# Performance work log

Hardware: AMD Instinct MI355X
Metric: run time of the kernel (lower is better)

The kernel has to match this reference:

```python
import jax, jax.numpy as jnp
import numpy as np

B, S, E, H = 4, 2048, 1024, 16
DK = E // H

def setup_inputs() -> dict:
    key = jax.random.key(0)
    ks = jax.random.split(key, 5)
    scale = 1.0 / np.sqrt(E)
    return {
        "x":  jax.random.normal(ks[0], (B, S, E), dtype=jnp.float32),
        "Wq": jax.random.normal(ks[1], (E, E), dtype=jnp.float32) * scale,
        "Wk": jax.random.normal(ks[2], (E, E), dtype=jnp.float32) * scale,
        "Wv": jax.random.normal(ks[3], (E, E), dtype=jnp.float32) * scale,
        "Wo": jax.random.normal(ks[4], (E, E), dtype=jnp.float32) * scale,
    }

def reference(x, Wq, Wk, Wv, Wo):
    b, s, e = x.shape
    # nn.Linear (no bias): y = x @ W.T
    def split_heads(t):  # (b, s, e) -> (b, H, s, DK)
        return t.reshape(b, s, H, DK).transpose(0, 2, 1, 3)
    Q = split_heads(x @ Wq.T)
    K = split_heads(x @ Wk.T)
    V = split_heads(x @ Wv.T)
    scores = jnp.einsum('bhqd,bhkd->bhqk', Q, K) / jnp.sqrt(jnp.float32(DK))
    attn = jax.nn.softmax(scores, axis=-1)  # dropout p=0.0 -> identity
    ctx = jnp.einsum('bhqk,bhkd->bhqd', attn, V)
    concat = ctx.transpose(0, 2, 1, 3).reshape(b, s, e)
    return concat @ Wo.T
```

## Files before the change

### kernel.cpp

```cpp
#include <hip/hip_runtime.h>


typedef __bf16 bf16x8 __attribute__((ext_vector_type(8)));
typedef __bf16 bf16x4 __attribute__((ext_vector_type(4)));
typedef float floatx4 __attribute__((ext_vector_type(4)));

#define GLOAD_LDS16(gp, lp) __builtin_amdgcn_global_load_lds( \
    (const __attribute__((address_space(1))) unsigned int*)(gp), \
    (__attribute__((address_space(3))) unsigned int*)(lp), 16, 0, 0)

__global__ __launch_bounds__(256) void cvt_x(const float4* __restrict__ s,
                                             bf16x4* __restrict__ d, int n4) {
    int i = blockIdx.x * 256 + threadIdx.x;
    if (i < n4) {
        float4 v = s[i];
        bf16x4 o = { (__bf16)v.x, (__bf16)v.y, (__bf16)v.z, (__bf16)v.w };
        d[i] = o;
    }
}

__global__ __launch_bounds__(256) void cvt_w(const float4* __restrict__ Wq,
                                             const float4* __restrict__ Wk,
                                             const float4* __restrict__ Wv,
                                             const float4* __restrict__ Wo,
                                             bf16x4* __restrict__ oq, bf16x4* __restrict__ ok,
                                             bf16x4* __restrict__ ov, bf16x4* __restrict__ oo,
                                             float qscale) {
    int y = blockIdx.y;
    const float4* s = (y == 0) ? Wq : (y == 1) ? Wk : (y == 2) ? Wv : Wo;
    bf16x4* d = (y == 0) ? oq : (y == 1) ? ok : (y == 2) ? ov : oo;
    float scale = (y == 0) ? qscale : 1.0f;
    int i = blockIdx.x * 256 + threadIdx.x;
    float4 v = s[i];
    bf16x4 o = { (__bf16)(v.x * scale), (__bf16)(v.y * scale),
                 (__bf16)(v.z * scale), (__bf16)(v.w * scale) };
    d[i] = o;
}


__device__ __forceinline__ void gemm_stage(const __bf16* __restrict__ A,
                                           const __bf16* __restrict__ W,
                                           __bf16* Asm, __bf16* Bsm,
                                           int bm, int bn, int k0, int w, int lane) {
#pragma unroll
    for (int j = 0; j < 2; ++j) {
        int base = j * 256 + w * 64;
        int flat = base + lane;
        int c = flat >> 7, r = flat & 127;
        GLOAD_LDS16(A + (size_t)(bm + r) * 1024 + k0 + c * 8, (char*)Asm + base * 16);
    }
#pragma unroll
    for (int j = 0; j < 4; ++j) {
        int base = j * 256 + w * 64;
        int flat = base + lane;
        int c = flat >> 8, r = flat & 255;
        GLOAD_LDS16(W + (size_t)(bn + r) * 1024 + k0 + c * 8, (char*)Bsm + base * 16);
    }
}

__device__ __forceinline__ void gemm_phase(const __bf16* __restrict__ A,
                                           const __bf16* __restrict__ W,
                                           const __bf16* Asm_r, const __bf16* Bsm_r,
                                           __bf16* Asm_s, __bf16* Bsm_s,
                                           int bm, int bn, int ks,
                                           int w, int lane, int quad, int l15,
                                           int wy, int wx,
                                           floatx4 acc[4][8]) {
    gemm_stage(A, W, Asm_s, Bsm_s, bm, bn, ks, w, lane);
    __builtin_amdgcn_sched_barrier(0);
    asm volatile("s_waitcnt vmcnt(6)" ::: "memory");
    __builtin_amdgcn_s_barrier();
    __builtin_amdgcn_sched_barrier(0);

    bf16x8 af[4], bf[8];
#pragma unroll
    for (int mt = 0; mt < 4; ++mt)
        af[mt] = *(const bf16x8*)(Asm_r + (quad * 128 + wy * 64 + mt * 16 + l15) * 8);
#pragma unroll
    for (int nt = 0; nt < 8; ++nt)
        bf[nt] = *(const bf16x8*)(Bsm_r + (quad * 256 + wx * 128 + nt * 16 + l15) * 8);
#pragma unroll
    for (int mt = 0; mt < 4; ++mt)
#pragma unroll
        for (int nt = 0; nt < 8; ++nt)
            acc[mt][nt] = __builtin_amdgcn_mfma_f32_16x16x32_bf16(af[mt], bf[nt],
                                                                  acc[mt][nt], 0, 0, 0);
    __builtin_amdgcn_sched_barrier(0);
    __builtin_amdgcn_s_barrier();
}

__device__ __forceinline__ void gemm_mainloop2(const __bf16* __restrict__ A,
                                               const __bf16* __restrict__ W,
                                               __bf16* SM,
                                               int bm, int bn, int tid,
                                               floatx4 acc[4][8]) {
    const int w = tid >> 6, lane = tid & 63;
    const int quad = lane >> 4, l15 = lane & 15;
    const int wy = w >> 1, wx = w & 1;
    __bf16* Asm0 = SM;
    __bf16* Bsm0 = SM + 4096;
    __bf16* Asm1 = SM + 12288;
    __bf16* Bsm1 = SM + 16384;
#pragma unroll
    for (int i = 0; i < 4; ++i)
#pragma unroll
        for (int j = 0; j < 8; ++j) acc[i][j] = (floatx4){0.f, 0.f, 0.f, 0.f};

    gemm_stage(A, W, Asm0, Bsm0, bm, bn, 0, w, lane);

    for (int k0 = 0; k0 < 1024; k0 += 64) {
        gemm_phase(A, W, Asm0, Bsm0, Asm1, Bsm1, bm, bn, k0 + 32,
                   w, lane, quad, l15, wy, wx, acc);
        gemm_phase(A, W, Asm1, Bsm1, Asm0, Bsm0, bm, bn, k0 + 64,
                   w, lane, quad, l15, wy, wx, acc);
    }
    __syncthreads();
}

__global__ __launch_bounds__(256, 2) void gemm_qkv(const __bf16* __restrict__ A,
                                                   const __bf16* __restrict__ Wqb,
                                                   const __bf16* __restrict__ Wkb,
                                                   const __bf16* __restrict__ Wvb,
                                                   __bf16* __restrict__ Qg,
                                                   __bf16* __restrict__ Kg,
                                                   __bf16* __restrict__ Vtg) {
    __shared__ alignas(16) __bf16 SM[24576];
    const int sel = blockIdx.x >> 2;
    const __bf16* W = (sel == 0) ? Wqb : (sel == 1) ? Wkb : Wvb;
    __bf16* ob = (sel == 0) ? Qg : (sel == 1) ? Kg : Vtg;
    const int bm = blockIdx.y * 128, bn = (blockIdx.x & 3) * 256;
    const int tid = threadIdx.x;
    const int w = tid >> 6, lane = tid & 63;
    const int quad = lane >> 4, l15 = lane & 15;
    const int wy = w >> 1, wx = w & 1;

    floatx4 acc[4][8];
    gemm_mainloop2(A, W, SM, bm, bn, tid, acc);

    float* tb = (float*)SM + w * 272;
    const int rr = lane >> 2, c0 = (lane & 3) * 4;
#pragma unroll
    for (int mt = 0; mt < 4; ++mt)
#pragma unroll
        for (int nt = 0; nt < 8; ++nt) {
            if (sel == 2) {
#pragma unroll
                for (int r = 0; r < 4; ++r) tb[l15 * 17 + quad * 4 + r] = acc[mt][nt][r];
            } else {
#pragma unroll
                for (int r = 0; r < 4; ++r) tb[(quad * 4 + r) * 17 + l15] = acc[mt][nt][r];
            }
            float f0 = tb[rr * 17 + c0 + 0], f1 = tb[rr * 17 + c0 + 1];
            float f2 = tb[rr * 17 + c0 + 2], f3 = tb[rr * 17 + c0 + 3];
            bf16x4 pk = { (__bf16)f0, (__bf16)f1, (__bf16)f2, (__bf16)f3 };
            if (sel <= 1) {
                int m = bm + wy * 64 + mt * 16 + rr;
                int n0 = bn + wx * 128 + nt * 16 + c0;
                int bI = m >> 11, s = m & 2047, h = n0 >> 6, d0 = n0 & 63;
                *(bf16x4*)(ob + ((size_t)(bI * 16 + h) * 2048 + s) * 64 + d0) = pk;
            } else {
                int m0 = bm + wy * 64 + mt * 16 + c0;
                int n = bn + wx * 128 + nt * 16 + rr;
                int bI = m0 >> 11, s0 = m0 & 2047, h = n >> 6, d = n & 63;
                *(bf16x4*)(ob + ((size_t)(bI * 16 + h) * 64 + d) * 2048 + s0) = pk;
            }
        }
}

__global__ __launch_bounds__(256, 2) void gemm_out(const __bf16* __restrict__ A,
                                                   const __bf16* __restrict__ W,
                                                   float* __restrict__ of) {
    __shared__ alignas(16) __bf16 SM[24576];
    const int tid = threadIdx.x;
    const int lane = tid & 63, w = tid >> 6;
    const int quad = lane >> 4, l15 = lane & 15;
    const int wy = w >> 1, wx = w & 1;
    const int bm = blockIdx.y * 128, bn = blockIdx.x * 256;

    floatx4 acc[4][8];
    gemm_mainloop2(A, W, SM, bm, bn, tid, acc);

#pragma unroll
    for (int mt = 0; mt < 4; ++mt)
#pragma unroll
        for (int nt = 0; nt < 8; ++nt)
#pragma unroll
            for (int r = 0; r < 4; ++r) {
                int m = bm + wy * 64 + mt * 16 + quad * 4 + r;
                int n = bn + wx * 128 + nt * 16 + l15;
                of[(size_t)m * 1024 + n] = acc[mt][nt][r];
            }
}


__device__ __forceinline__ int paddr(int c, int row) {
    int r2 = row ^ (((row >> 3) & 1) << 1) ^ (c & 1);
    return (c * 32 + r2) * 16;
}

__global__ __launch_bounds__(256, 4) void attn_kernel(const __bf16* __restrict__ Qg,
                                                      const __bf16* __restrict__ Kg,
                                                      const __bf16* __restrict__ Vtg,
                                                      __bf16* __restrict__ ctxg) {
    __shared__ alignas(16) __bf16 Ksm[4096];
    __shared__ alignas(16) __bf16 Vsm[4096];
    __shared__ alignas(16) __bf16 Psm[8192];
    const int tid = threadIdx.x;
    const int w = tid >> 6, lane = tid & 63;
    const int quad = lane >> 4, l15 = lane & 15;
    const int qbase = blockIdx.x * 128;
    const int bh = blockIdx.y;

    char* Pw = (char*)Psm + w * 4096;

    bf16x8 qf[2][2];
#pragma unroll
    for (int mt = 0; mt < 2; ++mt) {
        const __bf16* qrow = Qg + ((size_t)bh * 2048 + qbase + w * 32 + mt * 16 + l15) * 64;
        qf[mt][0] = *(const bf16x8*)(qrow + quad * 8);
        qf[mt][1] = *(const bf16x8*)(qrow + 32 + quad * 8);
    }

    float l_p[2][4] = {{0.f, 0.f, 0.f, 0.f}, {0.f, 0.f, 0.f, 0.f}};
    floatx4 o[2][4];
#pragma unroll
    for (int mt = 0; mt < 2; ++mt)
#pragma unroll
        for (int dt = 0; dt < 4; ++dt) o[mt][dt] = (floatx4){0.f, 0.f, 0.f, 0.f};

    for (int kv = 0; kv < 32; ++kv) {
        const int kv0 = kv * 64;
        __syncthreads();
#pragma unroll
        for (int j = 0; j < 2; ++j) {
            int base = j * 256 + w * 64;
            int flat = base + lane;
            int c = flat >> 6, r = flat & 63;
            GLOAD_LDS16(Kg + ((size_t)bh * 2048 + kv0 + r) * 64 + c * 8, (char*)Ksm + base * 16);
            GLOAD_LDS16(Vtg + ((size_t)bh * 64 + r) * 2048 + kv0 + c * 8, (char*)Vsm + base * 16);
        }
        __syncthreads();

        floatx4 sa[2][4];
#pragma unroll
        for (int mt = 0; mt < 2; ++mt)
#pragma unroll
            for (int nt = 0; nt < 4; ++nt) sa[mt][nt] = (floatx4){0.f, 0.f, 0.f, 0.f};
#pragma unroll
        for (int nt = 0; nt < 4; ++nt) {
            bf16x8 kb0 = *(const bf16x8*)(Ksm + (quad * 64 + nt * 16 + l15) * 8);
            bf16x8 kb1 = *(const bf16x8*)(Ksm + ((4 + quad) * 64 + nt * 16 + l15) * 8);
#pragma unroll
            for (int mt = 0; mt < 2; ++mt) {
                sa[mt][nt] = __builtin_amdgcn_mfma_f32_16x16x32_bf16(qf[mt][0], kb0,
                                                                    sa[mt][nt], 0, 0, 0);
                sa[mt][nt] = __builtin_amdgcn_mfma_f32_16x16x32_bf16(qf[mt][1], kb1,
                                                                    sa[mt][nt], 0, 0, 0);
            }
        }

#pragma unroll
        for (int mt = 0; mt < 2; ++mt)
#pragma unroll
            for (int nt = 0; nt < 4; ++nt)
#pragma unroll
                for (int r = 0; r < 4; ++r) {
                    float p = __builtin_amdgcn_exp2f(sa[mt][nt][r]);
                    l_p[mt][r] += p;
                    unsigned u = __builtin_bit_cast(unsigned, p);
                    *(unsigned short*)(Pw + paddr(nt * 2 + (l15 >> 3),
                                                  mt * 16 + quad * 4 + r)
                                       + (l15 & 7) * 2) = (unsigned short)(u >> 16);
                }

#pragma unroll
        for (int kk = 0; kk < 2; ++kk) {
            bf16x8 pa0 = *(const bf16x8*)(Pw + paddr(kk * 4 + quad, l15));
            bf16x8 pa1 = *(const bf16x8*)(Pw + paddr(kk * 4 + quad, 16 + l15));
#pragma unroll
            for (int dt = 0; dt < 4; ++dt) {
                bf16x8 vb = *(const bf16x8*)(Vsm + ((kk * 4 + quad) * 64 + dt * 16 + l15) * 8);
                o[0][dt] = __builtin_amdgcn_mfma_f32_16x16x32_bf16(pa0, vb, o[0][dt], 0, 0, 0);
                o[1][dt] = __builtin_amdgcn_mfma_f32_16x16x32_bf16(pa1, vb, o[1][dt], 0, 0, 0);
            }
        }
    }

    __syncthreads();

    float inv[2][4];
#pragma unroll
    for (int mt = 0; mt < 2; ++mt)
#pragma unroll
        for (int r = 0; r < 4; ++r) {
            float t = l_p[mt][r];
            t += __shfl_xor(t, 1); t += __shfl_xor(t, 2);
            t += __shfl_xor(t, 4); t += __shfl_xor(t, 8);
            inv[mt][r] = 1.f / t;
        }

    float* tb = (float*)Ksm + w * 272;
    const int bI = bh >> 4, h = bh & 15;
    const int rr = lane >> 2, c0 = (lane & 3) * 4;
#pragma unroll
    for (int mt = 0; mt < 2; ++mt)
#pragma unroll
        for (int dt = 0; dt < 4; ++dt) {
#pragma unroll
            for (int r = 0; r < 4; ++r)
                tb[(quad * 4 + r) * 17 + l15] = o[mt][dt][r] * inv[mt][r];
            float f0 = tb[rr * 17 + c0 + 0], f1 = tb[rr * 17 + c0 + 1];
            float f2 = tb[rr * 17 + c0 + 2], f3 = tb[rr * 17 + c0 + 3];
            bf16x4 pk = { (__bf16)f0, (__bf16)f1, (__bf16)f2, (__bf16)f3 };
            *(bf16x4*)(ctxg + ((size_t)(bI * 2048 + qbase + w * 32 + mt * 16 + rr)) * 1024
                       + h * 64 + dt * 16 + c0) = pk;
        }
}

extern "C" void kernel_launch(void* const* d_in, const int* in_sizes, int n_in,
                              void* d_out, int out_size, void* d_ws, size_t ws_size,
                              hipStream_t stream) {
    const float* x  = (const float*)d_in[0];
    const float* Wq = (const float*)d_in[1];
    const float* Wk = (const float*)d_in[2];
    const float* Wv = (const float*)d_in[3];
    const float* Wo = (const float*)d_in[4];
    float* out = (float*)d_out;
    char* ws = (char*)d_ws;

    __bf16* xb  = (__bf16*)(ws);
    __bf16* wqb = (__bf16*)(ws + (16u << 20));
    __bf16* wkb = (__bf16*)(ws + (18u << 20));
    __bf16* wvb = (__bf16*)(ws + (20u << 20));
    __bf16* wob = (__bf16*)(ws + (22u << 20));
    __bf16* Qg  = (__bf16*)(ws + (24u << 20));
    __bf16* Kg  = (__bf16*)(ws + (40u << 20));
    __bf16* Vtg = (__bf16*)(ws + (56u << 20));
    __bf16* ctx = xb;

    const float qscale = 0.18033688011112042f;

    cvt_x<<<8192, 256, 0, stream>>>((const float4*)x, (bf16x4*)xb, 2097152);
    cvt_w<<<dim3(1024, 4), 256, 0, stream>>>((const float4*)Wq, (const float4*)Wk,
                                             (const float4*)Wv, (const float4*)Wo,
                                             (bf16x4*)wqb, (bf16x4*)wkb,
                                             (bf16x4*)wvb, (bf16x4*)wob, qscale);

    gemm_qkv<<<dim3(12, 64), 256, 0, stream>>>(xb, wqb, wkb, wvb, Qg, Kg, Vtg);

    attn_kernel<<<dim3(16, 64), 256, 0, stream>>>(Qg, Kg, Vtg, ctx);

    gemm_out<<<dim3(4, 64), 256, 0, stream>>>(ctx, wob, out);
}
```

Baseline: 310.9 us.

## Double-buffer K/V tiles in attention and remap blocks across XCDs

The attention kernel now uses two LDS buffers for K and V. Each iteration prefetches the next tile with async global-to-LDS loads while it computes on the current one, synchronised by a vmcnt wait and a raw s_barrier, replacing the load-then-sync loop. The grid is flattened to 1D and block indices are permuted so that the query blocks of one head are grouped onto the same XCD, which should improve L2 reuse of K/V. LDS use grows, so occupancy drops from 4 to 3 blocks per CU. The last phase issues a redundant wrap-around prefetch of tile 0.

Result: no change. 309.9 us (-0.3%).

```diff
diff --git a/kernel.cpp b/kernel.cpp
--- a/kernel.cpp
+++ b/kernel.cpp
@@ -198,18 +198,98 @@
     return (c * 32 + r2) * 16;
 }
 
-__global__ __launch_bounds__(256, 4) void attn_kernel(const __bf16* __restrict__ Qg,
+__device__ __forceinline__ void attn_stage(const __bf16* __restrict__ Kg,
+                                           const __bf16* __restrict__ Vtg,
+                                           __bf16* Ks, __bf16* Vs,
+                                           int bh, int kv0, int w, int lane) {
+#pragma unroll
+    for (int j = 0; j < 2; ++j) {
+        int base = j * 256 + w * 64;
+        int flat = base + lane;
+        int c = flat >> 6, r = flat & 63;
+        GLOAD_LDS16(Kg + ((size_t)bh * 2048 + kv0 + r) * 64 + c * 8, (char*)Ks + base * 16);
+        GLOAD_LDS16(Vtg + ((size_t)bh * 64 + r) * 2048 + kv0 + c * 8, (char*)Vs + base * 16);
+    }
+}
+
+__device__ __forceinline__ void attn_phase(const __bf16* __restrict__ Kg,
+                                           const __bf16* __restrict__ Vtg,
+                                           const __bf16* Ksr, const __bf16* Vsr,
+                                           __bf16* Kss, __bf16* Vss,
+                                           char* Pw, const bf16x8 qf[2][2],
+                                           int bh, int kv_next,
+                                           int w, int lane, int quad, int l15,
+                                           float l_p[2][4], floatx4 o[2][4]) {
+    attn_stage(Kg, Vtg, Kss, Vss, bh, kv_next * 64, w, lane);
+    __builtin_amdgcn_sched_barrier(0);
+    asm volatile("s_waitcnt vmcnt(4)" ::: "memory");
+    __builtin_amdgcn_s_barrier();
+    __builtin_amdgcn_sched_barrier(0);
+
+    floatx4 sa[2][4];
+#pragma unroll
+    for (int mt = 0; mt < 2; ++mt)
+#pragma unroll
+        for (int nt = 0; nt < 4; ++nt) sa[mt][nt] = (floatx4){0.f, 0.f, 0.f, 0.f};
+#pragma unroll
+    for (int nt = 0; nt < 4; ++nt) {
+        bf16x8 kb0 = *(const bf16x8*)(Ksr + (quad * 64 + nt * 16 + l15) * 8);
+        bf16x8 kb1 = *(const bf16x8*)(Ksr + ((4 + quad) * 64 + nt * 16 + l15) * 8);
+#pragma unroll
+        for (int mt = 0; mt < 2; ++mt) {
+            sa[mt][nt] = __builtin_amdgcn_mfma_f32_16x16x32_bf16(qf[mt][0], kb0,
+                                                                sa[mt][nt], 0, 0, 0);
+            sa[mt][nt] = __builtin_amdgcn_mfma_f32_16x16x32_bf16(qf[mt][1], kb1,
+                                                                sa[mt][nt], 0, 0, 0);
+        }
+    }
+
+#pragma unroll
+    for (int mt = 0; mt < 2; ++mt)
+#pragma unroll
+        for (int nt = 0; nt < 4; ++nt)
+#pragma unroll
+            for (int r = 0; r < 4; ++r) {
+                float p = __builtin_amdgcn_exp2f(sa[mt][nt][r]);
+                l_p[mt][r] += p;
+                unsigned u = __builtin_bit_cast(unsigned, p);
+                *(unsigned short*)(Pw + paddr(nt * 2 + (l15 >> 3),
+                                              mt * 16 + quad * 4 + r)
+                                   + (l15 & 7) * 2) = (unsigned short)(u >> 16);
+            }
+
+#pragma unroll
+    for (int kk = 0; kk < 2; ++kk) {
+        bf16x8 pa0 = *(const bf16x8*)(Pw + paddr(kk * 4 + quad, l15));
+        bf16x8 pa1 = *(const bf16x8*)(Pw + paddr(kk * 4 + quad, 16 + l15));
+#pragma unroll
+        for (int dt = 0; dt < 4; ++dt) {
+            bf16x8 vb = *(const bf16x8*)(Vsr + ((kk * 4 + quad) * 64 + dt * 16 + l15) * 8);
+            o[0][dt] = __builtin_amdgcn_mfma_f32_16x16x32_bf16(pa0, vb, o[0][dt], 0, 0, 0);
+            o[1][dt] = __builtin_amdgcn_mfma_f32_16x16x32_bf16(pa1, vb, o[1][dt], 0, 0, 0);
+        }
+    }
+    __builtin_amdgcn_sched_barrier(0);
+    __builtin_amdgcn_s_barrier();
+}
+
+__global__ __launch_bounds__(256, 3) void attn_kernel(const __bf16* __restrict__ Qg,
                                                       const __bf16* __restrict__ Kg,
                                                       const __bf16* __restrict__ Vtg,
                                                       __bf16* __restrict__ ctxg) {
-    __shared__ alignas(16) __bf16 Ksm[4096];
-    __shared__ alignas(16) __bf16 Vsm[4096];
+    __shared__ alignas(16) __bf16 Ksm0[4096];
+    __shared__ alignas(16) __bf16 Vsm0[4096];
+    __shared__ alignas(16) __bf16 Ksm1[4096];
+    __shared__ alignas(16) __bf16 Vsm1[4096];
     __shared__ alignas(16) __bf16 Psm[8192];
     const int tid = threadIdx.x;
     const int w = tid >> 6, lane = tid & 63;
     const int quad = lane >> 4, l15 = lane & 15;
-    const int qbase = blockIdx.x * 128;
-    const int bh = blockIdx.y;
+
+    const int orig = blockIdx.x;
+    const int wg = (orig & 7) * 128 + (orig >> 3);
+    const int qbase = (wg & 15) * 128;
+    const int bh = wg >> 4;
 
     char* Pw = (char*)Psm + w * 4096;
 
@@ -228,62 +308,13 @@
 #pragma unroll
         for (int dt = 0; dt < 4; ++dt) o[mt][dt] = (floatx4){0.f, 0.f, 0.f, 0.f};
 
-    for (int kv = 0; kv < 32; ++kv) {
-        const int kv0 = kv * 64;
-        __syncthreads();
-#pragma unroll
-        for (int j = 0; j < 2; ++j) {
-            int base = j * 256 + w * 64;
-            int flat = base + lane;
-            int c = flat >> 6, r = flat & 63;
-            GLOAD_LDS16(Kg + ((size_t)bh * 2048 + kv0 + r) * 64 + c * 8, (char*)Ksm + base * 16);
-            GLOAD_LDS16(Vtg + ((size_t)bh * 64 + r) * 2048 + kv0 + c * 8, (char*)Vsm + base * 16);
-        }
-        __syncthreads();
-
-        floatx4 sa[2][4];
-#pragma unroll
-        for (int mt = 0; mt < 2; ++mt)
-#pragma unroll
-            for (int nt = 0; nt < 4; ++nt) sa[mt][nt] = (floatx4){0.f, 0.f, 0.f, 0.f};
-#pragma unroll
-        for (int nt = 0; nt < 4; ++nt) {
-            bf16x8 kb0 = *(const bf16x8*)(Ksm + (quad * 64 + nt * 16 + l15) * 8);
-            bf16x8 kb1 = *(const bf16x8*)(Ksm + ((4 + quad) * 64 + nt * 16 + l15) * 8);
-#pragma unroll
-            for (int mt = 0; mt < 2; ++mt) {
-                sa[mt][nt] = __builtin_amdgcn_mfma_f32_16x16x32_bf16(qf[mt][0], kb0,
-                                                                    sa[mt][nt], 0, 0, 0);
-                sa[mt][nt] = __builtin_amdgcn_mfma_f32_16x16x32_bf16(qf[mt][1], kb1,
-                                                                    sa[mt][nt], 0, 0, 0);
-            }
-        }
-
-#pragma unroll
-        for (int mt = 0; mt < 2; ++mt)
-#pragma unroll
-            for (int nt = 0; nt < 4; ++nt)
-#pragma unroll
-                for (int r = 0; r < 4; ++r) {
-                    float p = __builtin_amdgcn_exp2f(sa[mt][nt][r]);
-                    l_p[mt][r] += p;
-                    unsigned u = __builtin_bit_cast(unsigned, p);
-                    *(unsigned short*)(Pw + paddr(nt * 2 + (l15 >> 3),
-                                                  mt * 16 + quad * 4 + r)
-                                       + (l15 & 7) * 2) = (unsigned short)(u >> 16);
-                }
-
-#pragma unroll
-        for (int kk = 0; kk < 2; ++kk) {
-            bf16x8 pa0 = *(const bf16x8*)(Pw + paddr(kk * 4 + quad, l15));
-            bf16x8 pa1 = *(const bf16x8*)(Pw + paddr(kk * 4 + quad, 16 + l15));
-#pragma unroll
-            for (int dt = 0; dt < 4; ++dt) {
-                bf16x8 vb = *(const bf16x8*)(Vsm + ((kk * 4 + quad) * 64 + dt * 16 + l15) * 8);
-                o[0][dt] = __builtin_amdgcn_mfma_f32_16x16x32_bf16(pa0, vb, o[0][dt], 0, 0, 0);
-                o[1][dt] = __builtin_amdgcn_mfma_f32_16x16x32_bf16(pa1, vb, o[1][dt], 0, 0, 0);
-            }
-        }
+    attn_stage(Kg, Vtg, Ksm0, Vsm0, bh, 0, w, lane);
+
+    for (int kv = 0; kv < 32; kv += 2) {
+        attn_phase(Kg, Vtg, Ksm0, Vsm0, Ksm1, Vsm1, Pw, qf, bh, kv + 1,
+                   w, lane, quad, l15, l_p, o);
+        attn_phase(Kg, Vtg, Ksm1, Vsm1, Ksm0, Vsm0, Pw, qf, bh, (kv + 2) & 31,
+                   w, lane, quad, l15, l_p, o);
     }
 
     __syncthreads();
@@ -299,7 +330,7 @@
             inv[mt][r] = 1.f / t;
         }
 
-    float* tb = (float*)Ksm + w * 272;
+    float* tb = (float*)Ksm0 + w * 272;
     const int bI = bh >> 4, h = bh & 15;
     const int rr = lane >> 2, c0 = (lane & 3) * 4;
 #pragma unroll
@@ -348,7 +379,7 @@
 
     gemm_qkv<<<dim3(12, 64), 256, 0, stream>>>(xb, wqb, wkb, wvb, Qg, Kg, Vtg);
 
-    attn_kernel<<<dim3(16, 64), 256, 0, stream>>>(Qg, Kg, Vtg, ctx);
+    attn_kernel<<<1024, 256, 0, stream>>>(Qg, Kg, Vtg, ctx);
 
     gemm_out<<<dim3(4, 64), 256, 0, stream>>>(ctx, wob, out);
 }
```
